# Optimization experiments

Measured on AMD Instinct MI355X. Metric: run time of the kernel, lower is better.

## Reference

```python
import jax, jax.numpy as jnp
import numpy as np

D = 2048      # d_model
H = 32        # n_heads
DS = 64       # d_state = d_model // n_heads
K = 4         # conv kernel size (hardcoded in module)
EPS = 1e-6


def setup_inputs() -> dict:
    key = jax.random.key(0)
    ks = jax.random.split(key, 8)
    B, L = 2, 4096
    s = lambda k, shp, sc: jax.random.normal(k, shp, dtype=jnp.float32) * sc
    return {
        "x": s(ks[0], (B, L, D), 1.0),
        "state": jnp.zeros((B, H, DS), jnp.float32),
        "norm_w": jnp.ones((D,), jnp.float32),
        "conv_w": s(ks[1], (D, K), 0.5),          # depthwise conv weight [d_model, K]
        "conv_b": s(ks[2], (D,), 0.1),
        "pp_w": s(ks[3], (D, 3 * H * DS), 0.02),  # param_proj (stored [in, out])
        "pp_b": jnp.zeros((3 * H * DS,), jnp.float32),
        "gp_w": s(ks[4], (D, D), 0.02),           # gate_proj
        "gp_b": jnp.zeros((D,), jnp.float32),
        "op_w": s(ks[5], (D, D), 0.02),           # out_proj
        "op_b": jnp.zeros((D,), jnp.float32),
    }


def reference(x, state, norm_w, conv_w, conv_b, pp_w, pp_b, gp_w, gp_b, op_w, op_b):
    B, L, Dm = x.shape
    # RMSNorm
    rms = jnp.sqrt(jnp.mean(x * x, axis=-1, keepdims=True) + EPS)
    xn = norm_w * x / rms
    # causal depthwise conv1d + SiLU (pad left K-1, valid cross-correlation)
    xp = jnp.pad(xn, ((0, 0), (K - 1, 0), (0, 0)))
    xc = conv_b + sum(xp[:, k:k + L, :] * conv_w[:, k] for k in range(K))
    xc = jax.nn.silu(xc)
    gate = jax.nn.sigmoid(xc @ gp_w + gp_b)                  # [B, L, D]
    p = (xn @ pp_w + pp_b).reshape(B, L, H, 3, DS)
    delta = jax.nn.sigmoid(p[..., 0, :])                     # [B, L, H, DS]
    Bm, Cm = p[..., 1, :], p[..., 2, :]
    # sequential recurrence h_t = delta_t * h_{t-1} + B_t, time-major scan
    dt = jnp.moveaxis(delta, 1, 0)                           # [L, B, H, DS]
    Bt = jnp.moveaxis(Bm, 1, 0)
    def step(h, db):
        d, b = db
        h = d * h + b
        return h, h
    h_last, hs = jax.lax.scan(step, state, (dt, Bt))         # hs: [L, B, H, DS]
    ssm = (jnp.moveaxis(Cm, 1, 0) * hs).reshape(L, B, Dm)
    ssm = jnp.moveaxis(ssm, 0, 1)                            # [B, L, D]
    mixed = gate * ssm + (1.0 - gate) * xn
    y = mixed @ op_w + op_b + x
    return y, h_last
```

## Files before the change

kernel.cpp:

```cpp
#include <hip/hip_runtime.h>
#include <math.h>

#define BB   2
#define LL   4096
#define DD   2048
#define HH   32
#define DSS  64
#define MM   (BB * LL)
#define N3   (3 * HH * DSS)
#define NCH  64
#define CLN  64
#define EPSF 1e-6f
#define GP_NB (DD / 128)
#define PP_NB (N3 / 128)
#define TR_NBX 320
#define TR_NBY (DD / 32)

typedef unsigned short bf16;
typedef __attribute__((ext_vector_type(8))) short bf16x8;
typedef __attribute__((ext_vector_type(4))) float f32x4;

__device__ __forceinline__ float bf2f(bf16 u) {
    union { unsigned int i; float f; } v;
    v.i = ((unsigned int)u) << 16;
    return v.f;
}
__device__ __forceinline__ bf16 f2bf(float f) {
    union { float f; unsigned int u; } v;
    v.f = f;
    unsigned int r = (v.u >> 16) & 1u;
    return (bf16)((v.u + 0x7fffu + r) >> 16);
}
__device__ __forceinline__ float sigmoidf_(float v) {
    return 1.0f / (1.0f + __expf(-v));
}
__device__ __forceinline__ void gload16(const void* g, void* l) {
    __builtin_amdgcn_global_load_lds(
        (const __attribute__((address_space(1))) void*)g,
        (__attribute__((address_space(3))) void*)l, 16, 0, 0);
}

__global__ __launch_bounds__(256) void rms_transpose(const float* __restrict__ x,
                                                     const float* __restrict__ w,
                                                     bf16* __restrict__ xn,
                                                     const float* __restrict__ gp_w,
                                                     const float* __restrict__ op_w,
                                                     const float* __restrict__ pp_w,
                                                     bf16* __restrict__ gp_wT,
                                                     bf16* __restrict__ op_wT,
                                                     bf16* __restrict__ pp_wT) {
    __shared__ float sh[32 * 33];
    int t = threadIdx.x;
    if (blockIdx.x < MM) {
        int row = blockIdx.x;
        const float4* x4 = (const float4*)(x + (size_t)row * DD);
        ushort4* o4 = (ushort4*)(xn + (size_t)row * DD);
        const float4* w4 = (const float4*)w;
        float4 v0 = x4[t], v1 = x4[t + 256];
        float ss = v0.x * v0.x + v0.y * v0.y + v0.z * v0.z + v0.w * v0.w +
                   v1.x * v1.x + v1.y * v1.y + v1.z * v1.z + v1.w * v1.w;
#pragma unroll
        for (int off = 32; off >= 1; off >>= 1) ss += __shfl_down(ss, off, 64);
        if ((t & 63) == 0) sh[t >> 6] = ss;
        __syncthreads();
        float tot = sh[0] + sh[1] + sh[2] + sh[3];
        float inv = 1.0f / sqrtf(tot * (1.0f / DD) + EPSF);
        float4 wa = w4[t], wb = w4[t + 256];
        ushort4 r0, r1;
        r0.x = f2bf(v0.x * inv * wa.x); r0.y = f2bf(v0.y * inv * wa.y);
        r0.z = f2bf(v0.z * inv * wa.z); r0.w = f2bf(v0.w * inv * wa.w);
        r1.x = f2bf(v1.x * inv * wb.x); r1.y = f2bf(v1.y * inv * wb.y);
        r1.z = f2bf(v1.z * inv * wb.z); r1.w = f2bf(v1.w * inv * wb.w);
        o4[t] = r0; o4[t + 256] = r1;
    } else {
        int id = blockIdx.x - MM;
        int bx = id % TR_NBX;
        int k0 = (id / TR_NBX) << 5;
        const float* W; bf16* WT; int Ndim;
        if (bx < 64)       { W = gp_w; WT = gp_wT; Ndim = DD; }
        else if (bx < 128) { W = op_w; WT = op_wT; Ndim = DD; bx -= 64; }
        else               { W = pp_w; WT = pp_wT; Ndim = N3; bx -= 128; }
        int n0 = bx << 5;
        float (*tl)[33] = (float (*)[33])sh;
        int tx = t & 31, ty = t >> 5;
#pragma unroll
        for (int i = 0; i < 32; i += 8)
            tl[ty + i][tx] = W[(size_t)(k0 + ty + i) * Ndim + n0 + tx];
        __syncthreads();
        int tx2 = t & 15, ty2 = t >> 4;
#pragma unroll
        for (int i = 0; i < 32; i += 16) {
            int n = ty2 + i;
            ushort2 v = { f2bf(tl[tx2 * 2][n]), f2bf(tl[tx2 * 2 + 1][n]) };
            *(ushort2*)&WT[(size_t)(n0 + n) * DD + k0 + tx2 * 2] = v;
        }
    }
}

#define CONV_LC 16
__global__ __launch_bounds__(256) void conv_silu_kernel(const bf16* __restrict__ xn,
                                                        const float* __restrict__ cw,
                                                        const float* __restrict__ cb,
                                                        bf16* __restrict__ xc) {
    int b = blockIdx.z;
    int l0 = blockIdx.x * CONV_LC;
    int d0 = blockIdx.y * 1024 + threadIdx.x * 4;
    float4 w[4];
    float bias[4];
#pragma unroll
    for (int j = 0; j < 4; ++j) {
        w[j] = ((const float4*)cw)[d0 + j];
        bias[j] = cb[d0 + j];
    }
    float win[3][4];
#pragma unroll
    for (int k = 0; k < 3; ++k) {
        int l = l0 - 3 + k;
        if (l >= 0) {
            ushort4 v = *(const ushort4*)&xn[((size_t)b * LL + l) * DD + d0];
            win[k][0] = bf2f(v.x); win[k][1] = bf2f(v.y);
            win[k][2] = bf2f(v.z); win[k][3] = bf2f(v.w);
        } else {
            win[k][0] = win[k][1] = win[k][2] = win[k][3] = 0.0f;
        }
    }
    size_t off = ((size_t)b * LL + l0) * DD + d0;
#pragma unroll 4
    for (int i = 0; i < CONV_LC; ++i) {
        ushort4 v = *(const ushort4*)&xn[off];
        float cur[4] = {bf2f(v.x), bf2f(v.y), bf2f(v.z), bf2f(v.w)};
        ushort4 o;
#pragma unroll
        for (int j = 0; j < 4; ++j) {
            float acc = bias[j] + win[0][j] * w[j].x + win[1][j] * w[j].y +
                        win[2][j] * w[j].z + cur[j] * w[j].w;
            float s = acc * sigmoidf_(acc);
            ((unsigned short*)&o)[j] = f2bf(s);
        }
        *(ushort4*)&xc[off] = o;
#pragma unroll
        for (int j = 0; j < 4; ++j) {
            win[0][j] = win[1][j]; win[1][j] = win[2][j]; win[2][j] = cur[j];
        }
        off += DD;
    }
}

template <int EPI, typename OutT>
__device__ __forceinline__ void gemm_tile(const bf16* __restrict__ A,
                                          const bf16* __restrict__ Bt,
                                          const float* __restrict__ bias,
                                          const float* __restrict__ add,
                                          OutT* __restrict__ out,
                                          int Ndim, int m0, int n0,
                                          bf16* As, bf16* Bs) {
    const int tid  = threadIdx.x;
    const int wave = tid >> 6;
    const int lane = tid & 63;
    const int sr = lane >> 3;
    const int gcol = ((lane & 7) ^ sr) << 3;
    const bf16* gA[4];
    const bf16* gB[4];
    bf16* lA[4];
    bf16* lB[4];
#pragma unroll
    for (int p = 0; p < 4; ++p) {
        int c = wave * 4 + p;
        gA[p] = A  + (size_t)(m0 + c * 8 + sr) * DD + gcol;
        gB[p] = Bt + (size_t)(n0 + c * 8 + sr) * DD + gcol;
        lA[p] = As + c * 512 + lane * 8;
        lB[p] = Bs + c * 512 + lane * 8;
    }
    const int wm = (wave >> 1) << 6;
    const int wn = (wave & 1) << 6;
    const int fr = lane & 15;
    const int kg = lane >> 4;
    const int f7 = fr & 7;

    f32x4 acc[4][4] = {};
    for (int k0 = 0; k0 < DD; k0 += 64) {
        __syncthreads();
#pragma unroll
        for (int p = 0; p < 4; ++p) {
            gload16(gA[p] + k0, lA[p]);
            gload16(gB[p] + k0, lB[p]);
        }
        __syncthreads();
#pragma unroll
        for (int ks = 0; ks < 2; ++ks) {
            bf16x8 af[4], bf_[4];
#pragma unroll
            for (int i = 0; i < 4; ++i) {
                int gq = (((ks << 2) | kg) ^ f7) << 3;
                af[i]  = *(const bf16x8*)&As[(wm + i * 16 + fr) * 64 + gq];
                bf_[i] = *(const bf16x8*)&Bs[(wn + i * 16 + fr) * 64 + gq];
            }
#pragma unroll
            for (int i = 0; i < 4; ++i)
#pragma unroll
                for (int j = 0; j < 4; ++j)
                    acc[i][j] = __builtin_amdgcn_mfma_f32_16x16x32_bf16(
                        af[i], bf_[j], acc[i][j], 0, 0, 0);
        }
    }
    const int baseRow = m0 + wm + kg * 4;
    const int baseCol = n0 + wn + fr;
#pragma unroll
    for (int i = 0; i < 4; ++i) {
#pragma unroll
        for (int r = 0; r < 4; ++r) {
            int m = baseRow + i * 16 + r;
            size_t rowoff = (size_t)m * Ndim + baseCol;
#pragma unroll
            for (int j = 0; j < 4; ++j) {
                float v = acc[i][j][r] + bias[baseCol + j * 16];
                if (EPI == 1) v = sigmoidf_(v);
                if (EPI == 2) v += add[rowoff + j * 16];
                if constexpr (sizeof(OutT) == 4)
                    ((float*)out)[rowoff + j * 16] = v;
                else
                    ((bf16*)out)[rowoff + j * 16] = f2bf(v);
            }
        }
    }
}

__global__ __launch_bounds__(256) void gemm_gateproj(const bf16* __restrict__ xc,
                                                     const bf16* __restrict__ gp_wT,
                                                     const float* __restrict__ gp_b,
                                                     bf16* __restrict__ gate,
                                                     const bf16* __restrict__ xn,
                                                     const bf16* __restrict__ pp_wT,
                                                     const float* __restrict__ pp_b,
                                                     bf16* __restrict__ p) {
    __shared__ __align__(16) bf16 As[128 * 64];
    __shared__ __align__(16) bf16 Bs[128 * 64];
    const int m0 = blockIdx.y << 7;
    if (blockIdx.x < GP_NB) {
        gemm_tile<1, bf16>(xc, gp_wT, gp_b, nullptr, gate, DD,
                           m0, blockIdx.x << 7, As, Bs);
    } else {
        gemm_tile<0, bf16>(xn, pp_wT, pp_b, nullptr, p, N3,
                           m0, (blockIdx.x - GP_NB) << 7, As, Bs);
    }
}

__global__ __launch_bounds__(256) void gemm_out(const bf16* __restrict__ mixed,
                                                const bf16* __restrict__ op_wT,
                                                const float* __restrict__ op_b,
                                                const float* __restrict__ x,
                                                float* __restrict__ y) {
    __shared__ __align__(16) bf16 As[128 * 64];
    __shared__ __align__(16) bf16 Bs[128 * 64];
    gemm_tile<2, float>(mixed, op_wT, op_b, x, y, DD,
                        blockIdx.y << 7, blockIdx.x << 7, As, Bs);
}


__global__ __launch_bounds__(256) void scan_phase1(const bf16* __restrict__ p,
                                                   float* __restrict__ cA,
                                                   float* __restrict__ cB) {
    int c = blockIdx.x, b = blockIdx.z, s = threadIdx.x & 63;
    int h = blockIdx.y * 4 + (threadIdx.x >> 6);
    size_t base = ((size_t)(b * LL + c * CLN)) * N3 + h * (3 * DSS) + s;
    float a = 1.0f, bb = 0.0f;
#pragma unroll 8
    for (int i = 0; i < CLN; ++i) {
        float d = sigmoidf_(bf2f(p[base]));
        float Bv = bf2f(p[base + DSS]);
        a *= d;
        bb = d * bb + Bv;
        base += N3;
    }
    int idx = ((b * HH + h) * NCH + c) * DSS + s;
    cA[idx] = a;
    cB[idx] = bb;
}

__global__ __launch_bounds__(256) void scan_phase3(const bf16* __restrict__ p,
                                                   const float* __restrict__ cA,
                                                   const float* __restrict__ cB,
                                                   const float* __restrict__ state,
                                                   const bf16* __restrict__ gate,
                                                   const bf16* __restrict__ xn,
                                                   bf16* __restrict__ mixed,
                                                   float* __restrict__ hlast) {
    int c = blockIdx.x, b = blockIdx.z, s = threadIdx.x & 63;
    int h = blockIdx.y * 4 + (threadIdx.x >> 6);
    float hp = state[(b * HH + h) * DSS + s];
    int cbase = ((b * HH + h) * NCH) * DSS + s;
    for (int cc = 0; cc < c; ++cc)
        hp = cA[cbase + cc * DSS] * hp + cB[cbase + cc * DSS];
    size_t prow = ((size_t)(b * LL + c * CLN)) * N3 + h * (3 * DSS) + s;
    size_t grow = ((size_t)(b * LL + c * CLN)) * DD + h * DSS + s;
#pragma unroll 4
    for (int i = 0; i < CLN; ++i) {
        float d = sigmoidf_(bf2f(p[prow]));
        float Bv = bf2f(p[prow + DSS]);
        float Cv = bf2f(p[prow + 2 * DSS]);
        hp = d * hp + Bv;
        float ssm = Cv * hp;
        float g = bf2f(gate[grow]);
        float xv = bf2f(xn[grow]);
        mixed[grow] = f2bf(g * ssm + (1.0f - g) * xv);
        prow += N3;
        grow += DD;
    }
    if (c == NCH - 1) hlast[(b * HH + h) * DSS + s] = hp;
}

extern "C" void kernel_launch(void* const* d_in, const int* in_sizes, int n_in,
                              void* d_out, int out_size, void* d_ws, size_t ws_size,
                              hipStream_t stream) {
    const float* x      = (const float*)d_in[0];
    const float* state  = (const float*)d_in[1];
    const float* norm_w = (const float*)d_in[2];
    const float* conv_w = (const float*)d_in[3];
    const float* conv_b = (const float*)d_in[4];
    const float* pp_w   = (const float*)d_in[5];
    const float* pp_b   = (const float*)d_in[6];
    const float* gp_w   = (const float*)d_in[7];
    const float* gp_b   = (const float*)d_in[8];
    const float* op_w   = (const float*)d_in[9];
    const float* op_b   = (const float*)d_in[10];

    float* y     = (float*)d_out;
    float* hlast = y + (size_t)MM * DD;

    const size_t BHND = (size_t)BB * HH * NCH * DSS;
    char* ws = (char*)d_ws;
    bf16* xn    = (bf16*)ws;
    bf16* xcbuf = xn + (size_t)MM * DD;
    bf16* p     = xcbuf + (size_t)MM * DD;
    float* cA   = (float*)(p + (size_t)MM * N3);
    float* cB   = cA + BHND;
    bf16* gp_wT = (bf16*)(cB + BHND);
    bf16* op_wT = gp_wT + (size_t)DD * DD;
    bf16* gate  = (bf16*)y;
    bf16* pp_wT = gate + (size_t)MM * DD;
    bf16* mixed = xcbuf;

    rms_transpose<<<MM + TR_NBX * TR_NBY, 256, 0, stream>>>(
        x, norm_w, xn, gp_w, op_w, pp_w, gp_wT, op_wT, pp_wT);
    conv_silu_kernel<<<dim3(LL / CONV_LC, DD / 1024, BB), 256, 0, stream>>>(
        xn, conv_w, conv_b, xcbuf);
    gemm_gateproj<<<dim3(GP_NB + PP_NB, MM / 128), 256, 0, stream>>>(
        xcbuf, gp_wT, gp_b, gate, xn, pp_wT, pp_b, p);
    scan_phase1<<<dim3(NCH, HH / 4, BB), 256, 0, stream>>>(p, cA, cB);
    scan_phase3<<<dim3(NCH, HH / 4, BB), 256, 0, stream>>>(
        p, cA, cB, state, gate, xn, mixed, hlast);
    gemm_out<<<dim3(GP_NB, MM / 128), 256, 0, stream>>>(mixed, op_wT, op_b, x, y);
}
```

Before: 666.4 us.

## Reschedule kernels: fuse param-proj GEMM with conv, gate GEMM with scan phase 1

Regroups the pipeline. The param_proj GEMM now runs in the same launch as the depthwise conv, and the gate-proj GEMM now shares a launch with the chunk-summary scan, so work that does not depend on each other overlaps and two launches go away. The projection output is split into separate delta/B/C planes laid out like [M, D], which gives the scan kernels contiguous paired (ushort2) loads. The weight transpose uses 64-row tiles with ushort4 stores. The risks are tail imbalance in the heterogeneous grids and scattered bf16 stores in the projection epilogue.

Measured after the change: 668.9 us. No clear change (+0.4%).

```diff
diff --git a/kernel.cpp b/kernel.cpp
--- a/kernel.cpp
+++ b/kernel.cpp
@@ -13,8 +13,6 @@
 #define EPSF 1e-6f
 #define GP_NB (DD / 128)
 #define PP_NB (N3 / 128)
-#define TR_NBX 320
-#define TR_NBY (DD / 32)
 
 typedef unsigned short bf16;
 typedef __attribute__((ext_vector_type(8))) short bf16x8;
@@ -40,6 +38,9 @@
         (__attribute__((address_space(3))) void*)l, 16, 0, 0);
 }
 
+#define TR_GP 2048
+#define TR_OP 2048
+#define TR_PP 6144
 __global__ __launch_bounds__(256) void rms_transpose(const float* __restrict__ x,
                                                      const float* __restrict__ w,
                                                      bf16* __restrict__ xn,
@@ -49,7 +50,7 @@
                                                      bf16* __restrict__ gp_wT,
                                                      bf16* __restrict__ op_wT,
                                                      bf16* __restrict__ pp_wT) {
-    __shared__ float sh[32 * 33];
+    __shared__ float sh[64 * 33];
     int t = threadIdx.x;
     if (blockIdx.x < MM) {
         int row = blockIdx.x;
@@ -74,75 +75,28 @@
         o4[t] = r0; o4[t + 256] = r1;
     } else {
         int id = blockIdx.x - MM;
-        int bx = id % TR_NBX;
-        int k0 = (id / TR_NBX) << 5;
-        const float* W; bf16* WT; int Ndim;
-        if (bx < 64)       { W = gp_w; WT = gp_wT; Ndim = DD; }
-        else if (bx < 128) { W = op_w; WT = op_wT; Ndim = DD; bx -= 64; }
-        else               { W = pp_w; WT = pp_wT; Ndim = N3; bx -= 128; }
-        int n0 = bx << 5;
+        const float* W; bf16* WT; int Ndim, nblk, kblk;
+        if (id < TR_GP)               { W = gp_w; WT = gp_wT; Ndim = DD;
+                                        nblk = id & 63; kblk = id >> 6; }
+        else if (id < TR_GP + TR_OP)  { id -= TR_GP; W = op_w; WT = op_wT; Ndim = DD;
+                                        nblk = id & 63; kblk = id >> 6; }
+        else                          { id -= TR_GP + TR_OP; W = pp_w; WT = pp_wT; Ndim = N3;
+                                        nblk = id % 192; kblk = id / 192; }
+        int n0 = nblk << 5, k0 = kblk << 6;
         float (*tl)[33] = (float (*)[33])sh;
-        int tx = t & 31, ty = t >> 5;
-#pragma unroll
-        for (int i = 0; i < 32; i += 8)
-            tl[ty + i][tx] = W[(size_t)(k0 + ty + i) * Ndim + n0 + tx];
-        __syncthreads();
-        int tx2 = t & 15, ty2 = t >> 4;
+        int tn = t & 31, tk = t >> 5;
+#pragma unroll
+        for (int i = 0; i < 64; i += 8)
+            tl[tk + i][tn] = W[(size_t)(k0 + tk + i) * Ndim + n0 + tn];
+        __syncthreads();
+        int kq = (t & 15) << 2, tn2 = t >> 4;
 #pragma unroll
         for (int i = 0; i < 32; i += 16) {
-            int n = ty2 + i;
-            ushort2 v = { f2bf(tl[tx2 * 2][n]), f2bf(tl[tx2 * 2 + 1][n]) };
-            *(ushort2*)&WT[(size_t)(n0 + n) * DD + k0 + tx2 * 2] = v;
-        }
-    }
-}
-
-#define CONV_LC 16
-__global__ __launch_bounds__(256) void conv_silu_kernel(const bf16* __restrict__ xn,
-                                                        const float* __restrict__ cw,
-                                                        const float* __restrict__ cb,
-                                                        bf16* __restrict__ xc) {
-    int b = blockIdx.z;
-    int l0 = blockIdx.x * CONV_LC;
-    int d0 = blockIdx.y * 1024 + threadIdx.x * 4;
-    float4 w[4];
-    float bias[4];
-#pragma unroll
-    for (int j = 0; j < 4; ++j) {
-        w[j] = ((const float4*)cw)[d0 + j];
-        bias[j] = cb[d0 + j];
-    }
-    float win[3][4];
-#pragma unroll
-    for (int k = 0; k < 3; ++k) {
-        int l = l0 - 3 + k;
-        if (l >= 0) {
-            ushort4 v = *(const ushort4*)&xn[((size_t)b * LL + l) * DD + d0];
-            win[k][0] = bf2f(v.x); win[k][1] = bf2f(v.y);
-            win[k][2] = bf2f(v.z); win[k][3] = bf2f(v.w);
-        } else {
-            win[k][0] = win[k][1] = win[k][2] = win[k][3] = 0.0f;
-        }
-    }
-    size_t off = ((size_t)b * LL + l0) * DD + d0;
-#pragma unroll 4
-    for (int i = 0; i < CONV_LC; ++i) {
-        ushort4 v = *(const ushort4*)&xn[off];
-        float cur[4] = {bf2f(v.x), bf2f(v.y), bf2f(v.z), bf2f(v.w)};
-        ushort4 o;
-#pragma unroll
-        for (int j = 0; j < 4; ++j) {
-            float acc = bias[j] + win[0][j] * w[j].x + win[1][j] * w[j].y +
-                        win[2][j] * w[j].z + cur[j] * w[j].w;
-            float s = acc * sigmoidf_(acc);
-            ((unsigned short*)&o)[j] = f2bf(s);
-        }
-        *(ushort4*)&xc[off] = o;
-#pragma unroll
-        for (int j = 0; j < 4; ++j) {
-            win[0][j] = win[1][j]; win[1][j] = win[2][j]; win[2][j] = cur[j];
-        }
-        off += DD;
+            int n = tn2 + i;
+            ushort4 v = { f2bf(tl[kq + 0][n]), f2bf(tl[kq + 1][n]),
+                          f2bf(tl[kq + 2][n]), f2bf(tl[kq + 3][n]) };
+            *(ushort4*)&WT[(size_t)(n0 + n) * DD + k0 + kq] = v;
+        }
     }
 }
 
@@ -225,24 +179,238 @@
     }
 }
 
-__global__ __launch_bounds__(256) void gemm_gateproj(const bf16* __restrict__ xc,
-                                                     const bf16* __restrict__ gp_wT,
-                                                     const float* __restrict__ gp_b,
-                                                     bf16* __restrict__ gate,
-                                                     const bf16* __restrict__ xn,
-                                                     const bf16* __restrict__ pp_wT,
-                                                     const float* __restrict__ pp_b,
-                                                     bf16* __restrict__ p) {
+__device__ __forceinline__ void gemm_tile_proj(const bf16* __restrict__ A,
+                                               const bf16* __restrict__ Bt,
+                                               const float* __restrict__ bias,
+                                               bf16* __restrict__ dp,
+                                               bf16* __restrict__ Bp,
+                                               bf16* __restrict__ Cp,
+                                               int m0, int n0,
+                                               bf16* As, bf16* Bs) {
+    const int tid  = threadIdx.x;
+    const int wave = tid >> 6;
+    const int lane = tid & 63;
+    const int sr = lane >> 3;
+    const int gcol = ((lane & 7) ^ sr) << 3;
+    const bf16* gA[4];
+    const bf16* gB[4];
+    bf16* lA[4];
+    bf16* lB[4];
+#pragma unroll
+    for (int p = 0; p < 4; ++p) {
+        int c = wave * 4 + p;
+        gA[p] = A  + (size_t)(m0 + c * 8 + sr) * DD + gcol;
+        gB[p] = Bt + (size_t)(n0 + c * 8 + sr) * DD + gcol;
+        lA[p] = As + c * 512 + lane * 8;
+        lB[p] = Bs + c * 512 + lane * 8;
+    }
+    const int wm = (wave >> 1) << 6;
+    const int wn = (wave & 1) << 6;
+    const int fr = lane & 15;
+    const int kg = lane >> 4;
+    const int f7 = fr & 7;
+
+    f32x4 acc[4][4] = {};
+    for (int k0 = 0; k0 < DD; k0 += 64) {
+        __syncthreads();
+#pragma unroll
+        for (int p = 0; p < 4; ++p) {
+            gload16(gA[p] + k0, lA[p]);
+            gload16(gB[p] + k0, lB[p]);
+        }
+        __syncthreads();
+#pragma unroll
+        for (int ks = 0; ks < 2; ++ks) {
+            bf16x8 af[4], bf_[4];
+#pragma unroll
+            for (int i = 0; i < 4; ++i) {
+                int gq = (((ks << 2) | kg) ^ f7) << 3;
+                af[i]  = *(const bf16x8*)&As[(wm + i * 16 + fr) * 64 + gq];
+                bf_[i] = *(const bf16x8*)&Bs[(wn + i * 16 + fr) * 64 + gq];
+            }
+#pragma unroll
+            for (int i = 0; i < 4; ++i)
+#pragma unroll
+                for (int j = 0; j < 4; ++j)
+                    acc[i][j] = __builtin_amdgcn_mfma_f32_16x16x32_bf16(
+                        af[i], bf_[j], acc[i][j], 0, 0, 0);
+        }
+    }
+    const int baseRow = m0 + wm + kg * 4;
+    const int baseCol = n0 + wn + fr;
+    bf16* pl[4]; int po[4]; float bi[4];
+#pragma unroll
+    for (int j = 0; j < 4; ++j) {
+        int col = baseCol + j * 16;
+        int h = col / 192;
+        int rr = col - h * 192;
+        int jj = rr >> 6;
+        int s = rr & 63;
+        pl[j] = (jj == 0) ? dp : (jj == 1 ? Bp : Cp);
+        po[j] = h * DSS + s;
+        bi[j] = bias[col];
+    }
+#pragma unroll
+    for (int i = 0; i < 4; ++i) {
+#pragma unroll
+        for (int r = 0; r < 4; ++r) {
+            int m = baseRow + i * 16 + r;
+#pragma unroll
+            for (int j = 0; j < 4; ++j)
+                pl[j][(size_t)m * DD + po[j]] = f2bf(acc[i][j][r] + bi[j]);
+        }
+    }
+}
+
+#define CONV_LC 16
+#define CONV_NB 1024
+__global__ __launch_bounds__(256) void proj_conv(const bf16* __restrict__ xn,
+                                                 const bf16* __restrict__ pp_wT,
+                                                 const float* __restrict__ pp_b,
+                                                 bf16* __restrict__ dp,
+                                                 bf16* __restrict__ Bp,
+                                                 bf16* __restrict__ Cp,
+                                                 const float* __restrict__ cw,
+                                                 const float* __restrict__ cb,
+                                                 bf16* __restrict__ xc) {
     __shared__ __align__(16) bf16 As[128 * 64];
     __shared__ __align__(16) bf16 Bs[128 * 64];
-    const int m0 = blockIdx.y << 7;
-    if (blockIdx.x < GP_NB) {
+    int bid = blockIdx.x;
+    if (bid < PP_NB * (MM / 128)) {
+        int nblk = bid % PP_NB, mblk = bid / PP_NB;
+        gemm_tile_proj(xn, pp_wT, pp_b, dp, Bp, Cp, mblk << 7, nblk << 7, As, Bs);
+        return;
+    }
+    int cid = bid - PP_NB * (MM / 128);
+    int b = cid >> 9;
+    int rem = cid & 511;
+    int l0 = (rem & 255) * CONV_LC;
+    int d0 = (rem >> 8) * 1024 + threadIdx.x * 4;
+    float4 w[4];
+    float bias[4];
+#pragma unroll
+    for (int j = 0; j < 4; ++j) {
+        w[j] = ((const float4*)cw)[d0 + j];
+        bias[j] = cb[d0 + j];
+    }
+    float win[3][4];
+#pragma unroll
+    for (int k = 0; k < 3; ++k) {
+        int l = l0 - 3 + k;
+        if (l >= 0) {
+            ushort4 v = *(const ushort4*)&xn[((size_t)b * LL + l) * DD + d0];
+            win[k][0] = bf2f(v.x); win[k][1] = bf2f(v.y);
+            win[k][2] = bf2f(v.z); win[k][3] = bf2f(v.w);
+        } else {
+            win[k][0] = win[k][1] = win[k][2] = win[k][3] = 0.0f;
+        }
+    }
+    size_t off = ((size_t)b * LL + l0) * DD + d0;
+#pragma unroll 4
+    for (int i = 0; i < CONV_LC; ++i) {
+        ushort4 v = *(const ushort4*)&xn[off];
+        float cur[4] = {bf2f(v.x), bf2f(v.y), bf2f(v.z), bf2f(v.w)};
+        ushort4 o;
+#pragma unroll
+        for (int j = 0; j < 4; ++j) {
+            float acc = bias[j] + win[0][j] * w[j].x + win[1][j] * w[j].y +
+                        win[2][j] * w[j].z + cur[j] * w[j].w;
+            float s = acc * sigmoidf_(acc);
+            ((unsigned short*)&o)[j] = f2bf(s);
+        }
+        *(ushort4*)&xc[off] = o;
+#pragma unroll
+        for (int j = 0; j < 4; ++j) {
+            win[0][j] = win[1][j]; win[1][j] = win[2][j]; win[2][j] = cur[j];
+        }
+        off += DD;
+    }
+}
+
+#define SC1_NB (NCH * (HH / 8) * BB)
+__global__ __launch_bounds__(256) void gate_scan1(const bf16* __restrict__ xc,
+                                                  const bf16* __restrict__ gp_wT,
+                                                  const float* __restrict__ gp_b,
+                                                  bf16* __restrict__ gate,
+                                                  const bf16* __restrict__ dp,
+                                                  const bf16* __restrict__ Bpl,
+                                                  float* __restrict__ cA,
+                                                  float* __restrict__ cB) {
+    __shared__ __align__(16) bf16 As[128 * 64];
+    __shared__ __align__(16) bf16 Bs[128 * 64];
+    int bid = blockIdx.x;
+    if (bid < GP_NB * (MM / 128)) {
         gemm_tile<1, bf16>(xc, gp_wT, gp_b, nullptr, gate, DD,
-                           m0, blockIdx.x << 7, As, Bs);
-    } else {
-        gemm_tile<0, bf16>(xn, pp_wT, pp_b, nullptr, p, N3,
-                           m0, (blockIdx.x - GP_NB) << 7, As, Bs);
-    }
+                           (bid / GP_NB) << 7, (bid % GP_NB) << 7, As, Bs);
+        return;
+    }
+    int sid = bid - GP_NB * (MM / 128);
+    int c = sid & 63;
+    int rem = sid >> 6;
+    int hg = rem & 3, b = rem >> 2;
+    int t = threadIdx.x;
+    int h = hg * 8 + (t >> 5);
+    int so = (t & 31) * 2;
+    size_t base = ((size_t)(b * LL + c * CLN)) * DD + h * DSS + so;
+    float a0 = 1.0f, b0 = 0.0f, a1 = 1.0f, b1 = 0.0f;
+#pragma unroll 8
+    for (int i = 0; i < CLN; ++i) {
+        ushort2 dv = *(const ushort2*)&dp[base];
+        ushort2 bv = *(const ushort2*)&Bpl[base];
+        float d0 = sigmoidf_(bf2f(dv.x));
+        float d1 = sigmoidf_(bf2f(dv.y));
+        a0 *= d0; b0 = d0 * b0 + bf2f(bv.x);
+        a1 *= d1; b1 = d1 * b1 + bf2f(bv.y);
+        base += DD;
+    }
+    int idx = ((b * HH + h) * NCH + c) * DSS + so;
+    *(float2*)&cA[idx] = make_float2(a0, a1);
+    *(float2*)&cB[idx] = make_float2(b0, b1);
+}
+
+__global__ __launch_bounds__(256) void scan_phase3(const bf16* __restrict__ dp,
+                                                   const bf16* __restrict__ Bpl,
+                                                   const bf16* __restrict__ Cp,
+                                                   const float* __restrict__ cA,
+                                                   const float* __restrict__ cB,
+                                                   const float* __restrict__ state,
+                                                   const bf16* __restrict__ gate,
+                                                   const bf16* __restrict__ xn,
+                                                   bf16* __restrict__ mixed,
+                                                   float* __restrict__ hlast) {
+    int c = blockIdx.x, b = blockIdx.z;
+    int t = threadIdx.x;
+    int h = blockIdx.y * 8 + (t >> 5);
+    int so = (t & 31) * 2;
+    float2 hp = *(const float2*)&state[(b * HH + h) * DSS + so];
+    int cbase = ((b * HH + h) * NCH) * DSS + so;
+    for (int cc = 0; cc < c; ++cc) {
+        float2 a = *(const float2*)&cA[cbase + cc * DSS];
+        float2 bb = *(const float2*)&cB[cbase + cc * DSS];
+        hp.x = a.x * hp.x + bb.x;
+        hp.y = a.y * hp.y + bb.y;
+    }
+    size_t grow = ((size_t)(b * LL + c * CLN)) * DD + h * DSS + so;
+#pragma unroll 4
+    for (int i = 0; i < CLN; ++i) {
+        ushort2 dv = *(const ushort2*)&dp[grow];
+        ushort2 bv = *(const ushort2*)&Bpl[grow];
+        ushort2 cv = *(const ushort2*)&Cp[grow];
+        ushort2 gv = *(const ushort2*)&gate[grow];
+        ushort2 xv = *(const ushort2*)&xn[grow];
+        float d0 = sigmoidf_(bf2f(dv.x));
+        float d1 = sigmoidf_(bf2f(dv.y));
+        hp.x = d0 * hp.x + bf2f(bv.x);
+        hp.y = d1 * hp.y + bf2f(bv.y);
+        float g0 = bf2f(gv.x), g1 = bf2f(gv.y);
+        float m0 = g0 * (bf2f(cv.x) * hp.x) + (1.0f - g0) * bf2f(xv.x);
+        float m1 = g1 * (bf2f(cv.y) * hp.y) + (1.0f - g1) * bf2f(xv.y);
+        ushort2 o = { f2bf(m0), f2bf(m1) };
+        *(ushort2*)&mixed[grow] = o;
+        grow += DD;
+    }
+    if (c == NCH - 1)
+        *(float2*)&hlast[(b * HH + h) * DSS + so] = hp;
 }
 
 __global__ __launch_bounds__(256) void gemm_out(const bf16* __restrict__ mixed,
@@ -254,59 +422,6 @@
     __shared__ __align__(16) bf16 Bs[128 * 64];
     gemm_tile<2, float>(mixed, op_wT, op_b, x, y, DD,
                         blockIdx.y << 7, blockIdx.x << 7, As, Bs);
-}
-
-
-__global__ __launch_bounds__(256) void scan_phase1(const bf16* __restrict__ p,
-                                                   float* __restrict__ cA,
-                                                   float* __restrict__ cB) {
-    int c = blockIdx.x, b = blockIdx.z, s = threadIdx.x & 63;
-    int h = blockIdx.y * 4 + (threadIdx.x >> 6);
-    size_t base = ((size_t)(b * LL + c * CLN)) * N3 + h * (3 * DSS) + s;
-    float a = 1.0f, bb = 0.0f;
-#pragma unroll 8
-    for (int i = 0; i < CLN; ++i) {
-        float d = sigmoidf_(bf2f(p[base]));
-        float Bv = bf2f(p[base + DSS]);
-        a *= d;
-        bb = d * bb + Bv;
-        base += N3;
-    }
-    int idx = ((b * HH + h) * NCH + c) * DSS + s;
-    cA[idx] = a;
-    cB[idx] = bb;
-}
-
-__global__ __launch_bounds__(256) void scan_phase3(const bf16* __restrict__ p,
-                                                   const float* __restrict__ cA,
-                                                   const float* __restrict__ cB,
-                                                   const float* __restrict__ state,
-                                                   const bf16* __restrict__ gate,
-                                                   const bf16* __restrict__ xn,
-                                                   bf16* __restrict__ mixed,
-                                                   float* __restrict__ hlast) {
-    int c = blockIdx.x, b = blockIdx.z, s = threadIdx.x & 63;
-    int h = blockIdx.y * 4 + (threadIdx.x >> 6);
-    float hp = state[(b * HH + h) * DSS + s];
-    int cbase = ((b * HH + h) * NCH) * DSS + s;
-    for (int cc = 0; cc < c; ++cc)
-        hp = cA[cbase + cc * DSS] * hp + cB[cbase + cc * DSS];
-    size_t prow = ((size_t)(b * LL + c * CLN)) * N3 + h * (3 * DSS) + s;
-    size_t grow = ((size_t)(b * LL + c * CLN)) * DD + h * DSS + s;
-#pragma unroll 4
-    for (int i = 0; i < CLN; ++i) {
-        float d = sigmoidf_(bf2f(p[prow]));
-        float Bv = bf2f(p[prow + DSS]);
-        float Cv = bf2f(p[prow + 2 * DSS]);
-        hp = d * hp + Bv;
-        float ssm = Cv * hp;
-        float g = bf2f(gate[grow]);
-        float xv = bf2f(xn[grow]);
-        mixed[grow] = f2bf(g * ssm + (1.0f - g) * xv);
-        prow += N3;
-        grow += DD;
-    }
-    if (c == NCH - 1) hlast[(b * HH + h) * DSS + s] = hp;
 }
 
 extern "C" void kernel_launch(void* const* d_in, const int* in_sizes, int n_in,
@@ -331,8 +446,10 @@
     char* ws = (char*)d_ws;
     bf16* xn    = (bf16*)ws;
     bf16* xcbuf = xn + (size_t)MM * DD;
-    bf16* p     = xcbuf + (size_t)MM * DD;
-    float* cA   = (float*)(p + (size_t)MM * N3);
+    bf16* dp    = xcbuf + (size_t)MM * DD;
+    bf16* Bp    = dp + (size_t)MM * DD;
+    bf16* Cp    = Bp + (size_t)MM * DD;
+    float* cA   = (float*)(Cp + (size_t)MM * DD);
     float* cB   = cA + BHND;
     bf16* gp_wT = (bf16*)(cB + BHND);
     bf16* op_wT = gp_wT + (size_t)DD * DD;
@@ -340,14 +457,13 @@
     bf16* pp_wT = gate + (size_t)MM * DD;
     bf16* mixed = xcbuf;
 
-    rms_transpose<<<MM + TR_NBX * TR_NBY, 256, 0, stream>>>(
+    rms_transpose<<<MM + TR_GP + TR_OP + TR_PP, 256, 0, stream>>>(
         x, norm_w, xn, gp_w, op_w, pp_w, gp_wT, op_wT, pp_wT);
-    conv_silu_kernel<<<dim3(LL / CONV_LC, DD / 1024, BB), 256, 0, stream>>>(
-        xn, conv_w, conv_b, xcbuf);
-    gemm_gateproj<<<dim3(GP_NB + PP_NB, MM / 128), 256, 0, stream>>>(
-        xcbuf, gp_wT, gp_b, gate, xn, pp_wT, pp_b, p);
-    scan_phase1<<<dim3(NCH, HH / 4, BB), 256, 0, stream>>>(p, cA, cB);
-    scan_phase3<<<dim3(NCH, HH / 4, BB), 256, 0, stream>>>(
-        p, cA, cB, state, gate, xn, mixed, hlast);
+    proj_conv<<<PP_NB * (MM / 128) + CONV_NB, 256, 0, stream>>>(
+        xn, pp_wT, pp_b, dp, Bp, Cp, conv_w, conv_b, xcbuf);
+    gate_scan1<<<GP_NB * (MM / 128) + SC1_NB, 256, 0, stream>>>(
+        xcbuf, gp_wT, gp_b, gate, dp, Bp, cA, cB);
+    scan_phase3<<<dim3(NCH, HH / 8, BB), 256, 0, stream>>>(
+        dp, Bp, Cp, cA, cB, state, gate, xn, mixed, hlast);
     gemm_out<<<dim3(GP_NB, MM / 128), 256, 0, stream>>>(mixed, op_wT, op_b, x, y);
 }
```
